# Kernel tuning notes

Hardware: AMD Instinct MI355X
Metric: run time of the kernel (lower is better)

Reference implementation:

```python
import jax, jax.numpy as jnp
import numpy as np

B, C, H, W = 16, 256, 64, 64
NH = 4                      # num_heads
HD = C // NH                # head_dim = 64
G = 32                      # GroupNorm groups
EPS = 1e-5


def setup_inputs() -> dict:
    key = jax.random.key(0)
    ks = jax.random.split(key, 7)
    x = jax.random.normal(ks[0], (B, C, H, W), dtype=jnp.float32)
    gn_w = jnp.ones((C,), dtype=jnp.float32)
    gn_b = jnp.zeros((C,), dtype=jnp.float32)
    qkv_w = jax.random.normal(ks[1], (3 * C, C), dtype=jnp.float32) * 0.02
    qkv_b = jnp.zeros((3 * C,), dtype=jnp.float32)
    out_w = jax.random.normal(ks[2], (C, C), dtype=jnp.float32) * 0.02
    out_b = jnp.zeros((C,), dtype=jnp.float32)
    return {"x": x, "gn_w": gn_w, "gn_b": gn_b, "qkv_w": qkv_w,
            "qkv_b": qkv_b, "out_w": out_w, "out_b": out_b}


def _group_norm(x, w, b):
    # x: (B, C, H, W); normalize over each of G groups of channels (+ spatial)
    Bx, Cx, Hx, Wx = x.shape
    xr = x.reshape(Bx, G, -1)
    mean = xr.mean(axis=-1, keepdims=True)
    var = xr.var(axis=-1, keepdims=True)
    h = ((xr - mean) * jax.lax.rsqrt(var + EPS)).reshape(Bx, Cx, Hx, Wx)
    return h * w[None, :, None, None] + b[None, :, None, None]


def reference(x, gn_w, gn_b, qkv_w, qkv_b, out_w, out_b):
    Bx, Cx, Hx, Wx = x.shape
    N = Hx * Wx
    h = _group_norm(x, gn_w, gn_b)
    # 1x1 conv == channel matmul
    qkv = jnp.einsum('oc,bchw->bohw', qkv_w, h) + qkv_b[None, :, None, None]
    q, k, v = jnp.split(qkv, 3, axis=1)
    # b (h d) y x -> b h d n
    q = q.reshape(Bx, NH, HD, N)
    k = k.reshape(Bx, NH, HD, N)
    v = v.reshape(Bx, NH, HD, N)
    q = jax.nn.softmax(q, axis=-1)   # over spatial positions n
    k = jax.nn.softmax(k, axis=-2)   # over head_dim d
    # context = k @ v^T : (b,h,d,d)
    context = jnp.einsum('bhdn,bhen->bhde', k, v)
    # out = context^T @ q : (b,h,d,n)
    out = jnp.einsum('bhde,bhdn->bhen', context, q)
    out = out.reshape(Bx, Cx, Hx, Wx)
    out = jnp.einsum('oc,bchw->bohw', out_w, out) + out_b[None, :, None, None]
    return x + out
```

## Files before the change

### kernel.cpp

```cpp
#include <hip/hip_runtime.h>


typedef __bf16 bf16x8 __attribute__((ext_vector_type(8)));
typedef __bf16 bf16x4 __attribute__((ext_vector_type(4)));
typedef float  f32x4  __attribute__((ext_vector_type(4)));

__device__ __forceinline__ float wave_red_sum(float v) {
#pragma unroll
    for (int off = 32; off > 0; off >>= 1) v += __shfl_xor(v, off, 64);
    return v;
}
__device__ __forceinline__ float wave_red_max(float v) {
#pragma unroll
    for (int off = 32; off > 0; off >>= 1) v = fmaxf(v, __shfl_xor(v, off, 64));
    return v;
}

__global__ __launch_bounds__(256)
void gn_stats_kernel(const float* __restrict__ x, const float* __restrict__ gw,
                     const float* __restrict__ gb, float2* __restrict__ scsh)
{
    const int blk = blockIdx.x;
    const int b = blk >> 5, g = blk & 31;
    const int tid = threadIdx.x;
    const int lane = tid & 63, wid = tid >> 6;
    const size_t xbase = ((size_t)(b * 256 + g * 8)) * 4096;

    float s1 = 0.f, s2 = 0.f;
#pragma unroll
    for (int it = 0; it < 32; it++) {
        const int idx = (it * 256 + tid) * 4;
        const float4 v4 = *(const float4*)(x + xbase + idx);
        s1 += v4.x + v4.y + v4.z + v4.w;
        s2 += v4.x * v4.x + v4.y * v4.y + v4.z * v4.z + v4.w * v4.w;
    }
    __shared__ float red[8];
    float s1w = wave_red_sum(s1);
    float s2w = wave_red_sum(s2);
    if (lane == 0) { red[wid] = s1w; red[4 + wid] = s2w; }
    __syncthreads();
    const float mean = (red[0] + red[1] + red[2] + red[3]) * (1.0f / 32768.0f);
    const float ms   = (red[4] + red[5] + red[6] + red[7]) * (1.0f / 32768.0f);
    const float inv  = rsqrtf(fmaxf(ms - mean * mean, 0.f) + 1e-5f);

    if (tid < 8) {
        const int c = g * 8 + tid;
        const float sc = gw[c] * inv;
        const float sh = gb[c] - mean * sc;
        scsh[b * 256 + c] = make_float2(sc, sh);
    }
}

__global__ __launch_bounds__(256)
void wcast_kernel(const float* __restrict__ w, __bf16* __restrict__ wb)
{
    const int i = (blockIdx.x * 256 + threadIdx.x) * 4;
    const float4 f = *(const float4*)(w + i);
    bf16x4 t;
    t[0] = (__bf16)f.x; t[1] = (__bf16)f.y; t[2] = (__bf16)f.z; t[3] = (__bf16)f.w;
    *(bf16x4*)(wb + i) = t;
}

__global__ __launch_bounds__(256)
void gemm1_kernel(const __bf16* __restrict__ wbf,
                  const float* __restrict__ x,
                  const float* __restrict__ bias,
                  const float2* __restrict__ scsh,
                  __bf16* __restrict__ qkv)
{
    __shared__ __align__(16) char lds_a[8192];
    __shared__ __align__(16) char lds_b[8192];
    __shared__ float2 lscsh[256];

    const int tid  = threadIdx.x;
    const int lane = tid & 63;
    const int wid  = tid >> 6;
    const int quad = lane >> 4;
    const int tcol = lane & 15;
    const int wm   = (wid & 1) * 64;
    const int wn   = (wid >> 1) * 64;
    const int n0   = blockIdx.x * 128;
    const int m0   = blockIdx.y * 128;
    const int b    = n0 >> 12;
    const int nn   = n0 & 4095;

    lscsh[tid] = scsh[b * 256 + tid];

    const int sn  = tid & 127;
    const int sth = tid >> 7;
    const int am  = tid >> 1;
    const int ah  = tid & 1;

    f32x4 acc[4][4];
#pragma unroll
    for (int i = 0; i < 4; i++)
#pragma unroll
        for (int j = 0; j < 4; j++) acc[i][j] = {0.f, 0.f, 0.f, 0.f};

    const float* xcol = x + (size_t)b * 1048576 + nn + sn;
    const int aswz = (am >> 1) & 3;
    const int bswz = (sn >> 1) & 3;

    for (int kt = 0; kt < 256; kt += 32) {
        __syncthreads();
        {
            const __bf16* asrc = wbf + (m0 + am) * 256 + kt + ah * 16;
            const bf16x8 a0 = *(const bf16x8*)asrc;
            const bf16x8 a1 = *(const bf16x8*)(asrc + 8);
            *(bf16x8*)&lds_a[am * 64 + (((ah * 2)     + aswz) & 3) * 16] = a0;
            *(bf16x8*)&lds_a[am * 64 + (((ah * 2 + 1) + aswz) & 3) * 16] = a1;
        }
        {
            const float* xs = xcol + (size_t)(kt + sth * 16) * 4096;
            bf16x8 o0, o1;
#pragma unroll
            for (int j = 0; j < 16; j++) {
                const float2 ss = lscsh[kt + sth * 16 + j];
                const float f = xs[(size_t)j * 4096];
                const __bf16 v = (__bf16)(f * ss.x + ss.y);
                if (j < 8) o0[j] = v; else o1[j - 8] = v;
            }
            *(bf16x8*)&lds_b[sn * 64 + (((sth * 2)     + bswz) & 3) * 16] = o0;
            *(bf16x8*)&lds_b[sn * 64 + (((sth * 2 + 1) + bswz) & 3) * 16] = o1;
        }
        __syncthreads();

        bf16x8 af[4], bfr[4];
#pragma unroll
        for (int mi = 0; mi < 4; mi++) {
            const int m = wm + mi * 16 + tcol;
            af[mi] = *(const bf16x8*)&lds_a[m * 64 + ((quad + ((m >> 1) & 3)) & 3) * 16];
        }
#pragma unroll
        for (int ni = 0; ni < 4; ni++) {
            const int n = wn + ni * 16 + tcol;
            bfr[ni] = *(const bf16x8*)&lds_b[n * 64 + ((quad + ((n >> 1) & 3)) & 3) * 16];
        }
#pragma unroll
        for (int mi = 0; mi < 4; mi++)
#pragma unroll
            for (int ni = 0; ni < 4; ni++)
                acc[mi][ni] = __builtin_amdgcn_mfma_f32_16x16x32_bf16(
                    af[mi], bfr[ni], acc[mi][ni], 0, 0, 0);
    }

#pragma unroll
    for (int mi = 0; mi < 4; mi++) {
#pragma unroll
        for (int r = 0; r < 4; r++) {
            const int grow = m0 + wm + mi * 16 + quad * 4 + r;
            const float bv = bias[grow];
#pragma unroll
            for (int ni = 0; ni < 4; ni++) {
                const int gcol = n0 + wn + ni * 16 + tcol;
                qkv[(size_t)grow * 65536 + gcol] = (__bf16)(acc[mi][ni][r] + bv);
            }
        }
    }
}

__global__ __launch_bounds__(256)
void qstats_kernel(const __bf16* __restrict__ qkv, float2* __restrict__ qst)
{
    const int o = blockIdx.x >> 4;
    const int b = blockIdx.x & 15;
    const int tid = threadIdx.x;
    const int lane = tid & 63, wid = tid >> 6;
    const size_t base = (size_t)o * 65536 + (size_t)b * 4096;

    float v[16];
    float m = -INFINITY;
#pragma unroll
    for (int s = 0; s < 16; s++) {
        v[s] = (float)qkv[base + s * 256 + tid];
        m = fmaxf(m, v[s]);
    }
    __shared__ float red[4];
    float wmx = wave_red_max(m);
    if (lane == 0) red[wid] = wmx;
    __syncthreads();
    m = fmaxf(fmaxf(red[0], red[1]), fmaxf(red[2], red[3]));
    __syncthreads();
    float sum = 0.f;
#pragma unroll
    for (int s = 0; s < 16; s++) sum += __expf(v[s] - m);
    float wsm = wave_red_sum(sum);
    if (lane == 0) red[wid] = wsm;
    __syncthreads();
    if (tid == 0)
        qst[o * 16 + b] = make_float2(m, 1.0f / (red[0] + red[1] + red[2] + red[3]));
}

__global__ __launch_bounds__(256)
void ctx_mfma_kernel(const __bf16* __restrict__ qkv, float* __restrict__ ctx)
{
    const int bh = blockIdx.x >> 3, kc = blockIdx.x & 7;
    const int b = bh >> 2, hh = bh & 3;
    __shared__ __align__(16) __bf16 lk[64 * 72], lv[64 * 72];
    __shared__ float smax[4][64], ssum[4][64];
    const int tid = threadIdx.x;
    const int lane = tid & 63, wid = tid >> 6;
    const int quad = lane >> 4, tcol = lane & 15;
    const int eh = (wid & 1) * 32, dh = (wid >> 1) * 32;
    const int col = tid & 63, dq = tid >> 6;
    const int sd = tid >> 2, snn = (tid & 3) * 16;

    f32x4 acc[2][2];
#pragma unroll
    for (int i = 0; i < 2; i++)
#pragma unroll
        for (int j = 0; j < 2; j++) acc[i][j] = {0.f, 0.f, 0.f, 0.f};

    const size_t kbase = (size_t)(256 + hh * 64) * 65536 + (size_t)b * 4096 + kc * 512;
    const size_t vbase = (size_t)(512 + hh * 64) * 65536 + (size_t)b * 4096 + kc * 512;

    for (int nc = 0; nc < 512; nc += 64) {
        __syncthreads();
        {
            const __bf16* ks = qkv + kbase + (size_t)sd * 65536 + nc + snn;
            *(bf16x8*)&lk[sd * 72 + snn]     = *(const bf16x8*)ks;
            *(bf16x8*)&lk[sd * 72 + snn + 8] = *(const bf16x8*)(ks + 8);
            const __bf16* vs = qkv + vbase + (size_t)sd * 65536 + nc + snn;
            *(bf16x8*)&lv[sd * 72 + snn]     = *(const bf16x8*)vs;
            *(bf16x8*)&lv[sd * 72 + snn + 8] = *(const bf16x8*)(vs + 8);
        }
        __syncthreads();

        float kvv[16];
        float pm = -INFINITY;
#pragma unroll
        for (int i = 0; i < 16; i++) {
            kvv[i] = (float)lk[(dq * 16 + i) * 72 + col];
            pm = fmaxf(pm, kvv[i]);
        }
        smax[dq][col] = pm;
        __syncthreads();
        const float m = fmaxf(fmaxf(smax[0][col], smax[1][col]),
                              fmaxf(smax[2][col], smax[3][col]));
        float ps = 0.f;
#pragma unroll
        for (int i = 0; i < 16; i++) { kvv[i] = __expf(kvv[i] - m); ps += kvv[i]; }
        ssum[dq][col] = ps;
        __syncthreads();
        const float inv = 1.0f / (ssum[0][col] + ssum[1][col] + ssum[2][col] + ssum[3][col]);
#pragma unroll
        for (int i = 0; i < 16; i++)
            lk[(dq * 16 + i) * 72 + col] = (__bf16)(kvv[i] * inv);
        __syncthreads();

#pragma unroll
        for (int k2 = 0; k2 < 64; k2 += 32) {
            bf16x8 af[2], bfr[2];
#pragma unroll
            for (int mi = 0; mi < 2; mi++)
                af[mi] = *(const bf16x8*)&lv[(eh + mi * 16 + tcol) * 72 + k2 + quad * 8];
#pragma unroll
            for (int ni = 0; ni < 2; ni++)
                bfr[ni] = *(const bf16x8*)&lk[(dh + ni * 16 + tcol) * 72 + k2 + quad * 8];
#pragma unroll
            for (int mi = 0; mi < 2; mi++)
#pragma unroll
                for (int ni = 0; ni < 2; ni++)
                    acc[mi][ni] = __builtin_amdgcn_mfma_f32_16x16x32_bf16(
                        af[mi], bfr[ni], acc[mi][ni], 0, 0, 0);
        }
    }
    float* cb = ctx + (size_t)bh * 4096;
#pragma unroll
    for (int mi = 0; mi < 2; mi++)
#pragma unroll
        for (int ni = 0; ni < 2; ni++)
#pragma unroll
            for (int r = 0; r < 4; r++) {
                const int e = eh + mi * 16 + quad * 4 + r;
                const int d = dh + ni * 16 + tcol;
                atomicAdd(&cb[e * 64 + d], acc[mi][ni][r]);
            }
}

__global__ __launch_bounds__(256)
void w2_kernel(const float* __restrict__ ctx, const float* __restrict__ out_w,
               __bf16* __restrict__ w2)
{
    const int bh = blockIdx.x;
    const int b = bh >> 2, hh = bh & 3;
    const int tid = threadIdx.x;

    __shared__ __align__(16) float lctx[4096];
    const float* csrc = ctx + (size_t)bh * 4096;
#pragma unroll
    for (int i = 0; i < 4; i++)
        ((float4*)lctx)[tid + i * 256] = ((const float4*)csrc)[tid + i * 256];
    __syncthreads();

    float acc[64];
#pragma unroll
    for (int d = 0; d < 64; d++) acc[d] = 0.f;

    const float* wrow = out_w + (size_t)tid * 256 + hh * 64;
    for (int e = 0; e < 64; e++) {
        const float w = wrow[e];
#pragma unroll
        for (int d4 = 0; d4 < 64; d4 += 4) {
            const float4 c4 = *(const float4*)&lctx[e * 64 + d4];
            acc[d4 + 0] += w * c4.x;
            acc[d4 + 1] += w * c4.y;
            acc[d4 + 2] += w * c4.z;
            acc[d4 + 3] += w * c4.w;
        }
    }
    __bf16* dst = w2 + (size_t)b * 65536 + (size_t)tid * 256 + hh * 64;
#pragma unroll
    for (int d4 = 0; d4 < 64; d4 += 4) {
        bf16x4 t;
        t[0] = (__bf16)acc[d4 + 0]; t[1] = (__bf16)acc[d4 + 1];
        t[2] = (__bf16)acc[d4 + 2]; t[3] = (__bf16)acc[d4 + 3];
        *(bf16x4*)(dst + d4) = t;
    }
}

__global__ __launch_bounds__(256)
void gemm2_kernel(const __bf16* __restrict__ w2,
                  const __bf16* __restrict__ qkv,
                  const float2* __restrict__ qst,
                  const float* __restrict__ bias,
                  const float* __restrict__ xres,
                  float* __restrict__ out)
{
    __shared__ __align__(16) __bf16 lds_bt[128 * 264];
    __shared__ __align__(16) __bf16 lds_a[128 * 40];
    __shared__ float2 lqst[256];

    const int tid  = threadIdx.x;
    const int lane = tid & 63;
    const int wid  = tid >> 6;
    const int quad = lane >> 4;
    const int tcol = lane & 15;
    const int wm   = (wid & 1) * 64;
    const int wn   = (wid >> 1) * 64;
    const int n0   = blockIdx.x * 128;
    const int b    = n0 >> 12;

    lqst[tid] = qst[tid * 16 + b];
    __syncthreads();

    const int sn    = tid & 127;
    const int chalf = tid >> 7;
    const int swz   = (sn >> 3) & 3;
#pragma unroll
    for (int iter = 0; iter < 8; iter++) {
        const int cbase = iter * 32 + chalf * 16;
        bf16x8 o0, o1;
        const __bf16* qs = qkv + n0 + sn;
#pragma unroll
        for (int j = 0; j < 16; j++) {
            const int c = cbase + j;
            const float2 qq = lqst[c];
            const float f = (float)qs[(size_t)c * 65536];
            const __bf16 v = (__bf16)(__expf(f - qq.x) * qq.y);
            if (j < 8) o0[j] = v; else o1[j - 8] = v;
        }
        const int chunk = iter * 2 + chalf;
        const int chSw  = chunk ^ swz;
        __bf16* dst = &lds_bt[sn * 264 + chSw * 16];
        *(bf16x8*)dst       = o0;
        *(bf16x8*)(dst + 8) = o1;
    }

    const int arow = tid >> 1, k16 = (tid & 1) * 16;

    for (int mt = 0; mt < 2; mt++) {
        const int m0 = mt * 128;
        f32x4 acc[4][4];
#pragma unroll
        for (int i = 0; i < 4; i++)
#pragma unroll
            for (int j = 0; j < 4; j++) acc[i][j] = {0.f, 0.f, 0.f, 0.f};

        for (int kt = 0; kt < 256; kt += 32) {
            __syncthreads();
            {
                const __bf16* src = w2 + (size_t)b * 65536
                                  + (size_t)(m0 + arow) * 256 + kt + k16;
                const bf16x8 o0 = *(const bf16x8*)(src);
                const bf16x8 o1 = *(const bf16x8*)(src + 8);
                *(bf16x8*)&lds_a[arow * 40 + k16]     = o0;
                *(bf16x8*)&lds_a[arow * 40 + k16 + 8] = o1;
            }
            __syncthreads();

            bf16x8 af[4];
#pragma unroll
            for (int mi = 0; mi < 4; mi++)
                af[mi] = *(const bf16x8*)&lds_a[(wm + mi * 16 + tcol) * 40 + quad * 8];
            bf16x8 bfr[4];
#pragma unroll
            for (int ni = 0; ni < 4; ni++) {
                const int n = wn + ni * 16 + tcol;
                const int k = kt + quad * 8;
                const int chSw = (k >> 4) ^ ((n >> 3) & 3);
                bfr[ni] = *(const bf16x8*)&lds_bt[n * 264 + chSw * 16 + (k & 15)];
            }
#pragma unroll
            for (int mi = 0; mi < 4; mi++)
#pragma unroll
                for (int ni = 0; ni < 4; ni++)
                    acc[mi][ni] = __builtin_amdgcn_mfma_f32_16x16x32_bf16(
                        af[mi], bfr[ni], acc[mi][ni], 0, 0, 0);
        }

#pragma unroll
        for (int mi = 0; mi < 4; mi++) {
#pragma unroll
            for (int r = 0; r < 4; r++) {
                const int grow = m0 + wm + mi * 16 + quad * 4 + r;
                const float bv = bias[grow];
#pragma unroll
                for (int ni = 0; ni < 4; ni++) {
                    const int gcol = n0 + wn + ni * 16 + tcol;
                    const int n = gcol & 4095;
                    const size_t oidx = ((size_t)(b * 256 + grow)) * 4096 + n;
                    out[oidx] = acc[mi][ni][r] + bv + xres[oidx];
                }
            }
        }
    }
}

extern "C" void kernel_launch(void* const* d_in, const int* in_sizes, int n_in,
                              void* d_out, int out_size, void* d_ws, size_t ws_size,
                              hipStream_t stream)
{
    const float* x     = (const float*)d_in[0];
    const float* gn_w  = (const float*)d_in[1];
    const float* gn_b  = (const float*)d_in[2];
    const float* qkv_w = (const float*)d_in[3];
    const float* qkv_b = (const float*)d_in[4];
    const float* out_w = (const float*)d_in[5];
    const float* out_b = (const float*)d_in[6];
    float* out = (float*)d_out;

    char* ws = (char*)d_ws;
    __bf16* qkv  = (__bf16*)ws;
    float*  ctx  = (float*)(ws + (size_t)100663296);
    float2* scsh = (float2*)(ws + (size_t)101711872);
    float2* qst  = (float2*)(ws + (size_t)101744640);
    __bf16* wbf  = (__bf16*)(ws + (size_t)101777408);
    __bf16* w2   = qkv + (size_t)256 * 65536;

    hipMemsetAsync(ctx, 0, 262144 * sizeof(float), stream);
    gn_stats_kernel<<<512, 256, 0, stream>>>(x, gn_w, gn_b, scsh);
    wcast_kernel<<<192, 256, 0, stream>>>(qkv_w, wbf);
    gemm1_kernel<<<dim3(512, 6), 256, 0, stream>>>(wbf, x, qkv_b, scsh, qkv);
    qstats_kernel<<<4096, 256, 0, stream>>>(qkv, qst);
    ctx_mfma_kernel<<<512, 256, 0, stream>>>(qkv, ctx);
    w2_kernel<<<64, 256, 0, stream>>>(ctx, out_w, w2);
    gemm2_kernel<<<512, 256, 0, stream>>>(w2, qkv, qst, out_b, x, out);
}
```

Baseline: 279.2 us.

## Fuse q softmax partial stats into gemm1 epilogue and retile gemm2

Computes per-row partial max and sum-exp for the q rows inside the gemm1 epilogue and writes them to a partial buffer. A small reduce kernel then combines them, so the separate qstats pass that re-read all of q from memory goes away. gemm1's grid is transposed so M tiles vary fastest, giving L2 reuse of the x columns. gemm2 is restructured from one block handling both M tiles over a full-K q tile held in LDS into a 2D grid with per-K-step staging. That lowers LDS use and raises parallelism, but each q element's exp is now computed twice, once per M tile.

```diff
diff --git a/kernel.cpp b/kernel.cpp
--- a/kernel.cpp
+++ b/kernel.cpp
@@ -66,11 +66,13 @@
                   const float* __restrict__ x,
                   const float* __restrict__ bias,
                   const float2* __restrict__ scsh,
-                  __bf16* __restrict__ qkv)
+                  __bf16* __restrict__ qkv,
+                  float2* __restrict__ pbuf)
 {
     __shared__ __align__(16) char lds_a[8192];
     __shared__ __align__(16) char lds_b[8192];
     __shared__ float2 lscsh[256];
+    __shared__ float pm2[2][128], ps2[2][128];
 
     const int tid  = threadIdx.x;
     const int lane = tid & 63;
@@ -79,8 +81,8 @@
     const int tcol = lane & 15;
     const int wm   = (wid & 1) * 64;
     const int wn   = (wid >> 1) * 64;
-    const int n0   = blockIdx.x * 128;
-    const int m0   = blockIdx.y * 128;
+    const int m0   = blockIdx.x * 128;
+    const int n0   = blockIdx.y * 128;
     const int b    = n0 >> 12;
     const int nn   = n0 & 4095;
 
@@ -144,51 +146,66 @@
                     af[mi], bfr[ni], acc[mi][ni], 0, 0, 0);
     }
 
+    const bool qrows = (m0 < 256);
+
 #pragma unroll
     for (int mi = 0; mi < 4; mi++) {
 #pragma unroll
         for (int r = 0; r < 4; r++) {
             const int grow = m0 + wm + mi * 16 + quad * 4 + r;
             const float bv = bias[grow];
+            float v[4];
 #pragma unroll
             for (int ni = 0; ni < 4; ni++) {
                 const int gcol = n0 + wn + ni * 16 + tcol;
-                qkv[(size_t)grow * 65536 + gcol] = (__bf16)(acc[mi][ni][r] + bv);
-            }
-        }
-    }
-}
-
-__global__ __launch_bounds__(256)
-void qstats_kernel(const __bf16* __restrict__ qkv, float2* __restrict__ qst)
-{
-    const int o = blockIdx.x >> 4;
-    const int b = blockIdx.x & 15;
-    const int tid = threadIdx.x;
-    const int lane = tid & 63, wid = tid >> 6;
-    const size_t base = (size_t)o * 65536 + (size_t)b * 4096;
-
-    float v[16];
-    float m = -INFINITY;
-#pragma unroll
-    for (int s = 0; s < 16; s++) {
-        v[s] = (float)qkv[base + s * 256 + tid];
-        m = fmaxf(m, v[s]);
-    }
-    __shared__ float red[4];
-    float wmx = wave_red_max(m);
-    if (lane == 0) red[wid] = wmx;
-    __syncthreads();
-    m = fmaxf(fmaxf(red[0], red[1]), fmaxf(red[2], red[3]));
-    __syncthreads();
-    float sum = 0.f;
-#pragma unroll
-    for (int s = 0; s < 16; s++) sum += __expf(v[s] - m);
-    float wsm = wave_red_sum(sum);
-    if (lane == 0) red[wid] = wsm;
-    __syncthreads();
-    if (tid == 0)
-        qst[o * 16 + b] = make_float2(m, 1.0f / (red[0] + red[1] + red[2] + red[3]));
+                const __bf16 ob = (__bf16)(acc[mi][ni][r] + bv);
+                qkv[(size_t)grow * 65536 + gcol] = ob;
+                v[ni] = (float)ob;
+            }
+            if (qrows) {
+                float mx = fmaxf(fmaxf(v[0], v[1]), fmaxf(v[2], v[3]));
+                mx = fmaxf(mx, __shfl_xor(mx, 1, 64));
+                mx = fmaxf(mx, __shfl_xor(mx, 2, 64));
+                mx = fmaxf(mx, __shfl_xor(mx, 4, 64));
+                mx = fmaxf(mx, __shfl_xor(mx, 8, 64));
+                float s = __expf(v[0] - mx) + __expf(v[1] - mx)
+                        + __expf(v[2] - mx) + __expf(v[3] - mx);
+                s += __shfl_xor(s, 1, 64);
+                s += __shfl_xor(s, 2, 64);
+                s += __shfl_xor(s, 4, 64);
+                s += __shfl_xor(s, 8, 64);
+                if (tcol == 0) {
+                    const int lr = wm + mi * 16 + quad * 4 + r;
+                    pm2[wn >> 6][lr] = mx;
+                    ps2[wn >> 6][lr] = s;
+                }
+            }
+        }
+    }
+    if (qrows) {
+        __syncthreads();
+        if (tid < 128) {
+            const float ma = pm2[0][tid], mb = pm2[1][tid];
+            const float M = fmaxf(ma, mb);
+            const float S = ps2[0][tid] * __expf(ma - M) + ps2[1][tid] * __expf(mb - M);
+            pbuf[(size_t)(m0 + tid) * 512 + blockIdx.y] = make_float2(M, S);
+        }
+    }
+}
+
+__global__ __launch_bounds__(256)
+void qstats_reduce_kernel(const float2* __restrict__ pbuf, float2* __restrict__ qst)
+{
+    const int gid = blockIdx.x * 256 + threadIdx.x;
+    const int o = gid >> 4, b = gid & 15;
+    const float2* p = pbuf + (size_t)o * 512 + b * 32;
+    float M = -INFINITY;
+#pragma unroll
+    for (int t = 0; t < 32; t++) M = fmaxf(M, p[t].x);
+    float S = 0.f;
+#pragma unroll
+    for (int t = 0; t < 32; t++) S += p[t].y * __expf(p[t].x - M);
+    qst[o * 16 + b] = make_float2(M, 1.0f / S);
 }
 
 __global__ __launch_bounds__(256)
@@ -327,8 +344,8 @@
                   const float* __restrict__ xres,
                   float* __restrict__ out)
 {
-    __shared__ __align__(16) __bf16 lds_bt[128 * 264];
-    __shared__ __align__(16) __bf16 lds_a[128 * 40];
+    __shared__ __align__(16) char lds_a[8192];
+    __shared__ __align__(16) char lds_b[8192];
     __shared__ float2 lqst[256];
 
     const int tid  = threadIdx.x;
@@ -338,90 +355,83 @@
     const int tcol = lane & 15;
     const int wm   = (wid & 1) * 64;
     const int wn   = (wid >> 1) * 64;
-    const int n0   = blockIdx.x * 128;
+    const int m0   = blockIdx.x * 128;
+    const int n0   = blockIdx.y * 128;
     const int b    = n0 >> 12;
+    const int nn   = n0 & 4095;
 
     lqst[tid] = qst[tid * 16 + b];
-    __syncthreads();
-
-    const int sn    = tid & 127;
-    const int chalf = tid >> 7;
-    const int swz   = (sn >> 3) & 3;
-#pragma unroll
-    for (int iter = 0; iter < 8; iter++) {
-        const int cbase = iter * 32 + chalf * 16;
-        bf16x8 o0, o1;
-        const __bf16* qs = qkv + n0 + sn;
-#pragma unroll
-        for (int j = 0; j < 16; j++) {
-            const int c = cbase + j;
-            const float2 qq = lqst[c];
-            const float f = (float)qs[(size_t)c * 65536];
-            const __bf16 v = (__bf16)(__expf(f - qq.x) * qq.y);
-            if (j < 8) o0[j] = v; else o1[j - 8] = v;
-        }
-        const int chunk = iter * 2 + chalf;
-        const int chSw  = chunk ^ swz;
-        __bf16* dst = &lds_bt[sn * 264 + chSw * 16];
-        *(bf16x8*)dst       = o0;
-        *(bf16x8*)(dst + 8) = o1;
-    }
-
-    const int arow = tid >> 1, k16 = (tid & 1) * 16;
-
-    for (int mt = 0; mt < 2; mt++) {
-        const int m0 = mt * 128;
-        f32x4 acc[4][4];
-#pragma unroll
-        for (int i = 0; i < 4; i++)
-#pragma unroll
-            for (int j = 0; j < 4; j++) acc[i][j] = {0.f, 0.f, 0.f, 0.f};
-
-        for (int kt = 0; kt < 256; kt += 32) {
-            __syncthreads();
-            {
-                const __bf16* src = w2 + (size_t)b * 65536
-                                  + (size_t)(m0 + arow) * 256 + kt + k16;
-                const bf16x8 o0 = *(const bf16x8*)(src);
-                const bf16x8 o1 = *(const bf16x8*)(src + 8);
-                *(bf16x8*)&lds_a[arow * 40 + k16]     = o0;
-                *(bf16x8*)&lds_a[arow * 40 + k16 + 8] = o1;
-            }
-            __syncthreads();
-
-            bf16x8 af[4];
-#pragma unroll
-            for (int mi = 0; mi < 4; mi++)
-                af[mi] = *(const bf16x8*)&lds_a[(wm + mi * 16 + tcol) * 40 + quad * 8];
-            bf16x8 bfr[4];
+
+    const int sn  = tid & 127;
+    const int sth = tid >> 7;
+    const int am  = tid >> 1;
+    const int ah  = tid & 1;
+
+    f32x4 acc[4][4];
+#pragma unroll
+    for (int i = 0; i < 4; i++)
+#pragma unroll
+        for (int j = 0; j < 4; j++) acc[i][j] = {0.f, 0.f, 0.f, 0.f};
+
+    const __bf16* qcol = qkv + (size_t)b * 4096 + nn + sn;
+    const __bf16* abase = w2 + (size_t)b * 65536;
+    const int aswz = (am >> 1) & 3;
+    const int bswz = (sn >> 1) & 3;
+
+    for (int kt = 0; kt < 256; kt += 32) {
+        __syncthreads();
+        {
+            const __bf16* asrc = abase + (m0 + am) * 256 + kt + ah * 16;
+            const bf16x8 a0 = *(const bf16x8*)asrc;
+            const bf16x8 a1 = *(const bf16x8*)(asrc + 8);
+            *(bf16x8*)&lds_a[am * 64 + (((ah * 2)     + aswz) & 3) * 16] = a0;
+            *(bf16x8*)&lds_a[am * 64 + (((ah * 2 + 1) + aswz) & 3) * 16] = a1;
+        }
+        {
+            const __bf16* qs = qcol + (size_t)(kt + sth * 16) * 65536;
+            bf16x8 o0, o1;
+#pragma unroll
+            for (int j = 0; j < 16; j++) {
+                const float2 qq = lqst[kt + sth * 16 + j];
+                const float f = (float)qs[(size_t)j * 65536];
+                const __bf16 v = (__bf16)(__expf(f - qq.x) * qq.y);
+                if (j < 8) o0[j] = v; else o1[j - 8] = v;
+            }
+            *(bf16x8*)&lds_b[sn * 64 + (((sth * 2)     + bswz) & 3) * 16] = o0;
+            *(bf16x8*)&lds_b[sn * 64 + (((sth * 2 + 1) + bswz) & 3) * 16] = o1;
+        }
+        __syncthreads();
+
+        bf16x8 af[4], bfr[4];
+#pragma unroll
+        for (int mi = 0; mi < 4; mi++) {
+            const int m = wm + mi * 16 + tcol;
+            af[mi] = *(const bf16x8*)&lds_a[m * 64 + ((quad + ((m >> 1) & 3)) & 3) * 16];
+        }
+#pragma unroll
+        for (int ni = 0; ni < 4; ni++) {
+            const int n = wn + ni * 16 + tcol;
+            bfr[ni] = *(const bf16x8*)&lds_b[n * 64 + ((quad + ((n >> 1) & 3)) & 3) * 16];
+        }
+#pragma unroll
+        for (int mi = 0; mi < 4; mi++)
+#pragma unroll
+            for (int ni = 0; ni < 4; ni++)
+                acc[mi][ni] = __builtin_amdgcn_mfma_f32_16x16x32_bf16(
+                    af[mi], bfr[ni], acc[mi][ni], 0, 0, 0);
+    }
+
+#pragma unroll
+    for (int mi = 0; mi < 4; mi++) {
+#pragma unroll
+        for (int r = 0; r < 4; r++) {
+            const int grow = m0 + wm + mi * 16 + quad * 4 + r;
+            const float bv = bias[grow];
 #pragma unroll
             for (int ni = 0; ni < 4; ni++) {
-                const int n = wn + ni * 16 + tcol;
-                const int k = kt + quad * 8;
-                const int chSw = (k >> 4) ^ ((n >> 3) & 3);
-                bfr[ni] = *(const bf16x8*)&lds_bt[n * 264 + chSw * 16 + (k & 15)];
-            }
-#pragma unroll
-            for (int mi = 0; mi < 4; mi++)
-#pragma unroll
-                for (int ni = 0; ni < 4; ni++)
-                    acc[mi][ni] = __builtin_amdgcn_mfma_f32_16x16x32_bf16(
-                        af[mi], bfr[ni], acc[mi][ni], 0, 0, 0);
-        }
-
-#pragma unroll
-        for (int mi = 0; mi < 4; mi++) {
-#pragma unroll
-            for (int r = 0; r < 4; r++) {
-                const int grow = m0 + wm + mi * 16 + quad * 4 + r;
-                const float bv = bias[grow];
-#pragma unroll
-                for (int ni = 0; ni < 4; ni++) {
-                    const int gcol = n0 + wn + ni * 16 + tcol;
-                    const int n = gcol & 4095;
-                    const size_t oidx = ((size_t)(b * 256 + grow)) * 4096 + n;
-                    out[oidx] = acc[mi][ni][r] + bv + xres[oidx];
-                }
+                const int n = nn + wn + ni * 16 + tcol;
+                const size_t oidx = ((size_t)(b * 256 + grow)) * 4096 + n;
+                out[oidx] = acc[mi][ni][r] + bv + xres[oidx];
             }
         }
     }
@@ -446,14 +456,15 @@
     float2* scsh = (float2*)(ws + (size_t)101711872);
     float2* qst  = (float2*)(ws + (size_t)101744640);
     __bf16* wbf  = (__bf16*)(ws + (size_t)101777408);
+    float2* pbuf = (float2*)(ws + (size_t)102170624);
     __bf16* w2   = qkv + (size_t)256 * 65536;
 
     hipMemsetAsync(ctx, 0, 262144 * sizeof(float), stream);
     gn_stats_kernel<<<512, 256, 0, stream>>>(x, gn_w, gn_b, scsh);
     wcast_kernel<<<192, 256, 0, stream>>>(qkv_w, wbf);
-    gemm1_kernel<<<dim3(512, 6), 256, 0, stream>>>(wbf, x, qkv_b, scsh, qkv);
-    qstats_kernel<<<4096, 256, 0, stream>>>(qkv, qst);
+    gemm1_kernel<<<dim3(6, 512), 256, 0, stream>>>(wbf, x, qkv_b, scsh, qkv, pbuf);
+    qstats_reduce_kernel<<<16, 256, 0, stream>>>(pbuf, qst);
     ctx_mfma_kernel<<<512, 256, 0, stream>>>(qkv, ctx);
     w2_kernel<<<64, 256, 0, stream>>>(ctx, out_w, w2);
-    gemm2_kernel<<<512, 256, 0, stream>>>(w2, qkv, qst, out_b, x, out);
-}
+    gemm2_kernel<<<dim3(2, 512), 256, 0, stream>>>(w2, qkv, qst, out_b, x, out);
+}
```

Result: slower. 291.6 us (+4.5%).
